# Performance work log

Measured on AMD Instinct MI355X. Metric: run time of the kernel, lower is better.

## Reference

```python
import jax, jax.numpy as jnp
import numpy as np

GRAPH_SIZES = [864, 1728, 3456, 6912]
VERTEX_NUM = 6890
B, NZ, FC_DIM = 128, 128, 512
CH = [128, 128, 64, 32, 16]
EDGE_FACTOR = 6  # directed edges per node (triangle mesh)
LRELU = 0.2


def setup_inputs() -> dict:
    key = jax.random.key(0)
    ks = jax.random.split(key, 24)
    s = 0.02
    inp = {
        'x': jax.random.normal(ks[0], (B, NZ), jnp.float32),
        'fc_w1': s * jax.random.normal(ks[1], (NZ, FC_DIM), jnp.float32),
        'fc_b1': jnp.zeros((FC_DIM,), jnp.float32),
        'fc_w2': s * jax.random.normal(ks[2], (FC_DIM, GRAPH_SIZES[0] * CH[0]), jnp.float32),
        'fc_b2': jnp.zeros((GRAPH_SIZES[0] * CH[0],), jnp.float32),
    }
    # Chebyshev weights [K=3, C_in, C_out] per layer (+ final conv to 3)
    cio = [(CH[0], CH[1]), (CH[1], CH[2]), (CH[2], CH[3]), (CH[3], CH[4]), (CH[4], 3)]
    for i, (ci, co) in enumerate(cio):
        inp[f'W{i}'] = s * jax.random.normal(ks[3 + i], (3, ci, co), jnp.float32)
        inp[f'b{i}'] = jnp.zeros((co,), jnp.float32)
    # fixed edge lists per level
    for i, n in enumerate(GRAPH_SIZES):
        e = EDGE_FACTOR * n
        inp[f'edge{i}'] = jax.random.randint(ks[10 + i], (2, e), 0, n, dtype=jnp.int64)
    inp['perm_back'] = jax.random.randint(ks[20], (GRAPH_SIZES[-1],), 0, GRAPH_SIZES[-1], dtype=jnp.int64)
    return inp


def cheb_conv(x, edge_index, W, b, num_nodes):
    # PyG-style ChebConv with lambda_max=2: L_hat = L - I = -D^{-1/2} A D^{-1/2}
    src, dst = edge_index[0], edge_index[1]
    deg = jnp.zeros((num_nodes,), x.dtype).at[dst].add(jnp.ones(src.shape, x.dtype))
    dinv = jnp.where(deg > 0, 1.0 / jnp.sqrt(jnp.maximum(deg, 1.0)), 0.0)
    norm = -(dinv[src] * dinv[dst])  # [E]

    def prop(h):  # h: [B, N, C] -> L_hat @ h (gather + scatter-add over edges)
        msg = h[:, src, :] * norm[None, :, None]
        return jnp.zeros_like(h).at[:, dst, :].add(msg)

    Tx0 = x
    Tx1 = prop(Tx0)
    Tx2 = 2.0 * prop(Tx1) - Tx0
    out = (jnp.einsum('bnc,co->bno', Tx0, W[0])
           + jnp.einsum('bnc,co->bno', Tx1, W[1])
           + jnp.einsum('bnc,co->bno', Tx2, W[2]))
    return out + b


def lrelu(x):
    return jnp.where(x >= 0, x, LRELU * x)


def reference(x, fc_w1, fc_b1, fc_w2, fc_b2,
              W0, b0, W1, b1, W2, b2, W3, b3, W4, b4,
              edge0, edge1, edge2, edge3, perm_back):
    h = jax.nn.relu(x @ fc_w1 + fc_b1)
    h = h @ fc_w2 + fc_b2                      # dropout = identity (eval mode)
    h = h.reshape(h.shape[0], GRAPH_SIZES[0], -1)  # [B, 864, 128]
    edges = [edge0, edge1, edge2, edge3]
    Ws = [(W0, b0), (W1, b1), (W2, b2), (W3, b3)]
    for i in range(4):
        h = lrelu(cheb_conv(h, edges[i], Ws[i][0], Ws[i][1], GRAPH_SIZES[i]))
        if i < 3:
            h = jnp.repeat(h, 2, axis=1)       # Upsample(scale_factor=2) along nodes
    h = cheb_conv(h, edge3, W4, b4, GRAPH_SIZES[3])  # final conv to 3 coords
    h = h[:, perm_back, :]                      # perm_data gather
    return h[:, :VERTEX_NUM, :]
```

## Files before the change

### kernel.cpp

```cpp
#include <hip/hip_runtime.h>
#include <hip/hip_bf16.h>

#define DEVFN __device__ __forceinline__

__global__ void k_signal(float* out, float v) {
    if (threadIdx.x == 0 && blockIdx.x == 0) out[0] = v;
}

__global__ void k_detect64(const long long* __restrict__ p, int count, int* flag) {
    if (threadIdx.x == 0 && blockIdx.x == 0) {
        int ok = 1;
        for (int i = 0; i < count; i++) {
            long long v = p[i];
            if (v < 0 || v >= (1LL << 30)) { ok = 0; break; }
        }
        *flag = ok;
    }
}

__global__ __launch_bounds__(256) void k_cvt_idx(const void* __restrict__ p, int n,
                                                 const int* __restrict__ flag,
                                                 int* __restrict__ out) {
    int i = blockIdx.x * 256 + threadIdx.x;
    if (i >= n) return;
    if (*flag) out[i] = (int)((const long long*)p)[i];
    else       out[i] = ((const int*)p)[i];
}

__global__ __launch_bounds__(256) void k_fc1(const float* __restrict__ x,
                                             const float* __restrict__ w,
                                             const float* __restrict__ b,
                                             float* __restrict__ out) {
    int j = blockIdx.x * 256 + threadIdx.x;
    int m = blockIdx.y;
    float acc = b[j];
    const float* xr = x + m * 128;
    for (int k = 0; k < 128; k++)
        acc = fmaf(xr[k], w[k * 512 + j], acc);
    out[m * 512 + j] = fmaxf(acc, 0.f);
}

__global__ __launch_bounds__(256) void k_fc2_gemm3(const float* __restrict__ h1,
                                                   const float* __restrict__ w,
                                                   const float* __restrict__ bias,
                                                   float* __restrict__ out) {
    const int N = 110592, K = 512;
    constexpr int KT = 32, MT = 128, NT = 64, AST = 37;
    __shared__ float At[MT * AST];
    __shared__ float Bt[KT * NT];

    const int tid = threadIdx.x;
    const int cg = tid & 7;
    const int rg = tid >> 3;
    const int nbase = blockIdx.x * NT;
    const int c0 = cg * 8;

    float acc[4][8];
#pragma unroll
    for (int jj = 0; jj < 8; jj++) {
        float bj = bias[nbase + c0 + jj];
#pragma unroll
        for (int r = 0; r < 4; r++) acc[r][jj] = bj;
    }

    for (int k0 = 0; k0 < K; k0 += KT) {
        __syncthreads();
#pragma unroll
        for (int it = 0; it < 4; it++) {
            int idx = tid + it * 256;
            int row = idx >> 3, k4 = (idx & 7) * 4;
            float4 a = *(const float4*)(h1 + row * K + k0 + k4);
            float* dst = At + row * AST + k4;
            dst[0] = a.x; dst[1] = a.y; dst[2] = a.z; dst[3] = a.w;
        }
#pragma unroll
        for (int it = 0; it < 2; it++) {
            int idx = tid + it * 256;
            int kk = idx >> 4, c4 = (idx & 15) * 4;
            *(float4*)(Bt + kk * NT + c4) =
                *(const float4*)(w + (size_t)(k0 + kk) * N + nbase + c4);
        }
        __syncthreads();
#pragma unroll 4
        for (int k = 0; k < KT; k++) {
            float a0 = At[(rg * 4 + 0) * AST + k];
            float a1 = At[(rg * 4 + 1) * AST + k];
            float a2 = At[(rg * 4 + 2) * AST + k];
            float a3 = At[(rg * 4 + 3) * AST + k];
            float4 w0 = *(const float4*)(Bt + k * NT + c0);
            float4 w1 = *(const float4*)(Bt + k * NT + c0 + 4);
            float wv[8] = {w0.x, w0.y, w0.z, w0.w, w1.x, w1.y, w1.z, w1.w};
#pragma unroll
            for (int jj = 0; jj < 8; jj++) {
                acc[0][jj] = fmaf(a0, wv[jj], acc[0][jj]);
                acc[1][jj] = fmaf(a1, wv[jj], acc[1][jj]);
                acc[2][jj] = fmaf(a2, wv[jj], acc[2][jj]);
                acc[3][jj] = fmaf(a3, wv[jj], acc[3][jj]);
            }
        }
    }
#pragma unroll
    for (int r = 0; r < 4; r++) {
        int m = rg * 4 + r;
        float4 o0 = {acc[r][0], acc[r][1], acc[r][2], acc[r][3]};
        float4 o1 = {acc[r][4], acc[r][5], acc[r][6], acc[r][7]};
        *(float4*)(out + (size_t)m * N + nbase + c0) = o0;
        *(float4*)(out + (size_t)m * N + nbase + c0 + 4) = o1;
    }
}

__global__ __launch_bounds__(256) void k_zero_int(int* p, int n) {
    int i = blockIdx.x * 256 + threadIdx.x;
    if (i < n) p[i] = 0;
}

__global__ __launch_bounds__(256) void k_deg(const int* __restrict__ dst, int e,
                                             int* __restrict__ deg) {
    int i = blockIdx.x * 256 + threadIdx.x;
    if (i < e) atomicAdd(&deg[dst[i]], 1);
}

__global__ __launch_bounds__(256) void k_dinv(const int* __restrict__ deg,
                                              float* __restrict__ dinv, int n) {
    int i = blockIdx.x * 256 + threadIdx.x;
    if (i < n) dinv[i] = deg[i] > 0 ? 1.0f / sqrtf((float)deg[i]) : 0.0f;
}

__global__ __launch_bounds__(256) void k_scan(const int* __restrict__ deg,
                                              int* __restrict__ row_ptr, int n) {
    __shared__ int part[256];
    int tid = threadIdx.x;
    int per = (n + 255) / 256;
    int start = tid * per;
    int end = min(start + per, n);
    int s = 0;
    for (int i = start; i < end; i++) s += deg[i];
    part[tid] = s;
    __syncthreads();
    for (int off = 1; off < 256; off <<= 1) {
        int t = (tid >= off) ? part[tid - off] : 0;
        __syncthreads();
        part[tid] += t;
        __syncthreads();
    }
    int base = (tid == 0) ? 0 : part[tid - 1];
    int run = base;
    for (int i = start; i < end; i++) { row_ptr[i] = run; run += deg[i]; }
    if (tid == 255) row_ptr[n] = part[255];
}

__global__ __launch_bounds__(256) void k_fill(const int* __restrict__ src,
                                              const int* __restrict__ dst, int e,
                                              const int* __restrict__ row_ptr,
                                              int* __restrict__ cnt,
                                              const float* __restrict__ dinv,
                                              int* __restrict__ col, float* __restrict__ val) {
    int i = blockIdx.x * 256 + threadIdx.x;
    if (i >= e) return;
    int d = dst[i], s = src[i];
    int slot = row_ptr[d] + atomicAdd(&cnt[d], 1);
    col[slot] = s;
    val[slot] = -dinv[s] * dinv[d];
}

template <int CI, int MODE>
__global__ __launch_bounds__(256) void k_prop2(const float* __restrict__ h,
                                               const float* __restrict__ sub,
                                               const int* __restrict__ row_ptr,
                                               const int* __restrict__ col,
                                               const float* __restrict__ val,
                                               float* __restrict__ out, int n) {
    constexpr int C4 = CI / 4;
    constexpr int BY = 256 / C4;
    int c4 = threadIdx.x;
    int d = blockIdx.x;
    int b = blockIdx.y * BY + threadIdx.y;
    int p0 = row_ptr[d], p1 = row_ptr[d + 1];
    float4 acc = {0.f, 0.f, 0.f, 0.f};
    const float4* hb = (const float4*)h + (size_t)b * n * C4;
    for (int p = p0; p < p1; p++) {
        float vp = val[p];
        float4 hv = hb[(size_t)col[p] * C4 + c4];
        acc.x = fmaf(vp, hv.x, acc.x);
        acc.y = fmaf(vp, hv.y, acc.y);
        acc.z = fmaf(vp, hv.z, acc.z);
        acc.w = fmaf(vp, hv.w, acc.w);
    }
    size_t oi = ((size_t)b * n + d) * C4 + c4;
    if (MODE) {
        float4 s = ((const float4*)sub)[oi];
        acc.x = 2.f * acc.x - s.x;
        acc.y = 2.f * acc.y - s.y;
        acc.z = 2.f * acc.z - s.z;
        acc.w = 2.f * acc.w - s.w;
    }
    ((float4*)out)[oi] = acc;
}

template <int CI, int CO, bool REPEAT>
__global__ __launch_bounds__(256) void k_cheb_gemm3(const float* __restrict__ t0,
                                                    const float* __restrict__ t1,
                                                    const float* __restrict__ t2,
                                                    const float* __restrict__ W,
                                                    const float* __restrict__ bias,
                                                    float* __restrict__ out, int n) {
    constexpr int CGN = CO / 8;
    constexpr int MT = 1024 / CGN;
    constexpr int KT = 32, AST = 37;
    __shared__ float At[MT * AST];
    __shared__ float Wt_s[KT * CO];

    const int tid = threadIdx.x;
    const int cg = tid % CGN;
    const int rg = tid / CGN;
    const int m_base = blockIdx.x * MT;
    const int c0 = cg * 8;

    float acc[4][8];
#pragma unroll
    for (int jj = 0; jj < 8; jj++) {
        float bj = bias[c0 + jj];
#pragma unroll
        for (int r = 0; r < 4; r++) acc[r][jj] = bj;
    }

    const float* As[3] = {t0, t1, t2};
#pragma unroll 1
    for (int t = 0; t < 3; t++) {
        const float* A = As[t];
        const float* Wg = W + t * CI * CO;
#pragma unroll 1
        for (int k0 = 0; k0 < CI; k0 += KT) {
            __syncthreads();
#pragma unroll
            for (int it = 0; it < MT / 32; it++) {
                int idx = tid + it * 256;
                int row = idx >> 3, k4 = (idx & 7) * 4;
                float4 a = *(const float4*)(A + (size_t)(m_base + row) * CI + k0 + k4);
                float* dst = At + row * AST + k4;
                dst[0] = a.x; dst[1] = a.y; dst[2] = a.z; dst[3] = a.w;
            }
#pragma unroll
            for (int it = 0; it < (KT * CO) / 1024; it++) {
                int idx = tid + it * 256;
                int kk = idx / (CO / 4), c4 = (idx % (CO / 4)) * 4;
                *(float4*)(Wt_s + kk * CO + c4) =
                    *(const float4*)(Wg + (k0 + kk) * CO + c4);
            }
            __syncthreads();
#pragma unroll 4
            for (int k = 0; k < KT; k++) {
                float a0 = At[(rg * 4 + 0) * AST + k];
                float a1 = At[(rg * 4 + 1) * AST + k];
                float a2 = At[(rg * 4 + 2) * AST + k];
                float a3 = At[(rg * 4 + 3) * AST + k];
                float4 w0 = *(const float4*)(Wt_s + k * CO + c0);
                float4 w1 = *(const float4*)(Wt_s + k * CO + c0 + 4);
                float wv[8] = {w0.x, w0.y, w0.z, w0.w, w1.x, w1.y, w1.z, w1.w};
#pragma unroll
                for (int jj = 0; jj < 8; jj++) {
                    acc[0][jj] = fmaf(a0, wv[jj], acc[0][jj]);
                    acc[1][jj] = fmaf(a1, wv[jj], acc[1][jj]);
                    acc[2][jj] = fmaf(a2, wv[jj], acc[2][jj]);
                    acc[3][jj] = fmaf(a3, wv[jj], acc[3][jj]);
                }
            }
        }
    }

#pragma unroll
    for (int r = 0; r < 4; r++) {
        int m = m_base + rg * 4 + r;
#pragma unroll
        for (int jj = 0; jj < 8; jj++) {
            float v = acc[r][jj];
            acc[r][jj] = v >= 0.f ? v : 0.2f * v;
        }
        float4 o0 = {acc[r][0], acc[r][1], acc[r][2], acc[r][3]};
        float4 o1 = {acc[r][4], acc[r][5], acc[r][6], acc[r][7]};
        if (REPEAT) {
            int b = m / n, d = m - (m / n) * n;
            size_t ob = ((size_t)b * (2 * n) + 2 * d) * CO + c0;
            *(float4*)(out + ob) = o0;
            *(float4*)(out + ob + 4) = o1;
            *(float4*)(out + ob + CO) = o0;
            *(float4*)(out + ob + CO + 4) = o1;
        } else {
            *(float4*)(out + (size_t)m * CO + c0) = o0;
            *(float4*)(out + (size_t)m * CO + c0 + 4) = o1;
        }
    }
}

__global__ __launch_bounds__(256) void k_cheb_small(const float* __restrict__ t0,
                                                    const float* __restrict__ t1,
                                                    const float* __restrict__ t2,
                                                    const float* __restrict__ W,
                                                    const float* __restrict__ bias,
                                                    float* __restrict__ out) {
    constexpr int CI = 32, CO = 16, MT = 256, AST = 33;
    __shared__ float At[MT * AST];
    __shared__ float Ws[3 * CI * CO];

    const int tid = threadIdx.x;
    const int cg = tid & 1;
    const int rg = tid >> 1;
    const int c0 = cg * 8;
    const int m_base = blockIdx.x * MT;

    for (int i = tid; i < 384; i += 256)
        ((float4*)Ws)[i] = ((const float4*)W)[i];

    float acc[2][8];
#pragma unroll
    for (int jj = 0; jj < 8; jj++) {
        float bj = bias[c0 + jj];
        acc[0][jj] = bj; acc[1][jj] = bj;
    }

    const float* As[3] = {t0, t1, t2};
#pragma unroll 1
    for (int t = 0; t < 3; t++) {
        const float* A = As[t];
        __syncthreads();
#pragma unroll
        for (int it = 0; it < 8; it++) {
            int idx = tid + it * 256;
            int row = idx >> 3, k4 = (idx & 7) * 4;
            float4 a = *(const float4*)(A + (size_t)(m_base + row) * CI + k4);
            float* dst = At + row * AST + k4;
            dst[0] = a.x; dst[1] = a.y; dst[2] = a.z; dst[3] = a.w;
        }
        __syncthreads();
        const float* Wt = Ws + t * CI * CO;
#pragma unroll 8
        for (int k = 0; k < CI; k++) {
            float a0 = At[rg * AST + k];
            float a1 = At[(rg + 128) * AST + k];
            float4 w0 = *(const float4*)(Wt + k * CO + c0);
            float4 w1 = *(const float4*)(Wt + k * CO + c0 + 4);
            float wv[8] = {w0.x, w0.y, w0.z, w0.w, w1.x, w1.y, w1.z, w1.w};
#pragma unroll
            for (int jj = 0; jj < 8; jj++) {
                acc[0][jj] = fmaf(a0, wv[jj], acc[0][jj]);
                acc[1][jj] = fmaf(a1, wv[jj], acc[1][jj]);
            }
        }
    }

#pragma unroll
    for (int r = 0; r < 2; r++) {
        int m = m_base + rg + r * 128;
#pragma unroll
        for (int jj = 0; jj < 8; jj++) {
            float v = acc[r][jj];
            acc[r][jj] = v >= 0.f ? v : 0.2f * v;
        }
        float4 o0 = {acc[r][0], acc[r][1], acc[r][2], acc[r][3]};
        float4 o1 = {acc[r][4], acc[r][5], acc[r][6], acc[r][7]};
        *(float4*)(out + (size_t)m * CO + c0) = o0;
        *(float4*)(out + (size_t)m * CO + c0 + 4) = o1;
    }
}

__global__ __launch_bounds__(256) void k_final_conv(const float* __restrict__ t0,
                                                    const float* __restrict__ t1,
                                                    const float* __restrict__ t2,
                                                    const float* __restrict__ W,
                                                    const float* __restrict__ bias,
                                                    float* __restrict__ out, int M) {
    int m = blockIdx.x * 256 + threadIdx.x;
    if (m >= M) return;
    float a0 = bias[0], a1 = bias[1], a2 = bias[2];
    const float* hs[3] = {t0, t1, t2};
#pragma unroll
    for (int t = 0; t < 3; t++) {
        const float4* h4 = (const float4*)(hs[t] + (size_t)m * 16);
        const float* Wt = W + t * 48;
#pragma unroll
        for (int q = 0; q < 4; q++) {
            float4 hv = h4[q];
            const float* Wq = Wt + q * 12;
            a0 = fmaf(hv.x, Wq[0], a0); a1 = fmaf(hv.x, Wq[1], a1); a2 = fmaf(hv.x, Wq[2], a2);
            a0 = fmaf(hv.y, Wq[3], a0); a1 = fmaf(hv.y, Wq[4], a1); a2 = fmaf(hv.y, Wq[5], a2);
            a0 = fmaf(hv.z, Wq[6], a0); a1 = fmaf(hv.z, Wq[7], a1); a2 = fmaf(hv.z, Wq[8], a2);
            a0 = fmaf(hv.w, Wq[9], a0); a1 = fmaf(hv.w, Wq[10], a1); a2 = fmaf(hv.w, Wq[11], a2);
        }
    }
    out[(size_t)m * 3 + 0] = a0;
    out[(size_t)m * 3 + 1] = a1;
    out[(size_t)m * 3 + 2] = a2;
}

__global__ __launch_bounds__(256) void k_permute(const float* __restrict__ h,
                                                 const int* __restrict__ perm,
                                                 float* __restrict__ out) {
    const int V = 6890, N = 6912;
    int idx = blockIdx.x * 256 + threadIdx.x;
    if (idx >= 128 * V * 3) return;
    int c = idx % 3;
    int t = idx / 3;
    int v = t % V;
    int b = t / V;
    int p = perm[v];
    out[idx] = h[((size_t)b * N + p) * 3 + c];
}

extern "C" void kernel_launch(void* const* d_in, const int* in_sizes, int n_in,
                              void* d_out, int out_size, void* d_ws, size_t ws_size,
                              hipStream_t stream) {
    float* out = (float*)d_out;

    static const int SIZES[20] = {
        16384, 65536, 512, 56623104, 110592,
        49152, 128, 24576, 64, 6144, 32, 1536, 16, 144, 3,
        10368, 20736, 41472, 82944, 6912
    };
    const void* in[20];
    bool map_ok = (n_in == 20);
    if (map_ok) {
        for (int s = 0; s < 20; s++) {
            int found = -1;
            for (int i = 0; i < n_in; i++)
                if (in_sizes[i] == SIZES[s]) { found = i; break; }
            if (found < 0) { map_ok = false; break; }
            in[s] = d_in[found];
        }
    }
    if (!map_ok)
        for (int i = 0; i < 20 && i < n_in; i++) in[i] = d_in[i];

    const float* x     = (const float*)in[0];
    const float* fc_w1 = (const float*)in[1];
    const float* fc_b1 = (const float*)in[2];
    const float* fc_w2 = (const float*)in[3];
    const float* fc_b2 = (const float*)in[4];
    const float* W0 = (const float*)in[5];
    const float* b0 = (const float*)in[6];
    const float* W1 = (const float*)in[7];
    const float* b1 = (const float*)in[8];
    const float* W2 = (const float*)in[9];
    const float* b2 = (const float*)in[10];
    const float* W3 = (const float*)in[11];
    const float* b3 = (const float*)in[12];
    const float* W4 = (const float*)in[13];
    const float* b4 = (const float*)in[14];

    const size_t SZ = 28311552;
    float* ws = (float*)d_ws;
    float* buf0 = ws;
    float* buf1 = ws + SZ;
    float* buf2 = ws + 2 * SZ;
    float* buf3 = ws + 3 * SZ;
    float* h1   = ws + 4 * SZ;
    float* dinv = h1 + 65536;
    float* val  = dinv + 6912;
    int* ideg = (int*)(val + 41472);
    int* rowp = ideg + 6912;
    int* cnt  = rowp + 6913;
    int* col  = cnt + 6912;
    int* e0 = col + 41472;
    int* e1 = e0 + 10368;
    int* e2 = e1 + 20736;
    int* e3 = e2 + 41472;
    int* pm = e3 + 82944;
    int* flag = pm + 6912;
    size_t needed = (char*)(flag + 1) - (char*)d_ws;
    if (ws_size < needed) {
        k_signal<<<1, 64, 0, stream>>>(out, 1000.0f);
        return;
    }

    k_detect64<<<1, 64, 0, stream>>>((const long long*)in[15], 64, flag);
    k_cvt_idx<<<(10368 + 255) / 256, 256, 0, stream>>>(in[15], 10368, flag, e0);
    k_cvt_idx<<<(20736 + 255) / 256, 256, 0, stream>>>(in[16], 20736, flag, e1);
    k_cvt_idx<<<(41472 + 255) / 256, 256, 0, stream>>>(in[17], 41472, flag, e2);
    k_cvt_idx<<<(82944 + 255) / 256, 256, 0, stream>>>(in[18], 82944, flag, e3);
    k_cvt_idx<<<(6912 + 255) / 256, 256, 0, stream>>>(in[19], 6912, flag, pm);

    k_fc1<<<dim3(2, 128), 256, 0, stream>>>(x, fc_w1, fc_b1, h1);
    k_fc2_gemm3<<<1728, 256, 0, stream>>>(h1, fc_w2, fc_b2, buf0);

    auto build = [&](const int* edge, int e, int n) {
        int nb_n = (n + 255) / 256, nb_e = (e + 255) / 256;
        k_zero_int<<<nb_n, 256, 0, stream>>>(ideg, n);
        k_zero_int<<<nb_n, 256, 0, stream>>>(cnt, n);
        k_deg<<<nb_e, 256, 0, stream>>>(edge + e, e, ideg);
        k_dinv<<<nb_n, 256, 0, stream>>>(ideg, dinv, n);
        k_scan<<<1, 256, 0, stream>>>(ideg, rowp, n);
        k_fill<<<nb_e, 256, 0, stream>>>(edge, edge + e, e, rowp, cnt, dinv, col, val);
    };

    build(e0, 6 * 864, 864);
    k_prop2<128, 0><<<dim3(864, 16), dim3(32, 8), 0, stream>>>(buf0, buf0, rowp, col, val, buf1, 864);
    k_prop2<128, 1><<<dim3(864, 16), dim3(32, 8), 0, stream>>>(buf1, buf0, rowp, col, val, buf2, 864);
    k_cheb_gemm3<128, 128, true><<<1728, 256, 0, stream>>>(buf0, buf1, buf2, W0, b0, buf3, 864);

    build(e1, 6 * 1728, 1728);
    k_prop2<128, 0><<<dim3(1728, 16), dim3(32, 8), 0, stream>>>(buf3, buf3, rowp, col, val, buf1, 1728);
    k_prop2<128, 1><<<dim3(1728, 16), dim3(32, 8), 0, stream>>>(buf1, buf3, rowp, col, val, buf2, 1728);
    k_cheb_gemm3<128, 64, true><<<1728, 256, 0, stream>>>(buf3, buf1, buf2, W1, b1, buf0, 1728);

    build(e2, 6 * 3456, 3456);
    k_prop2<64, 0><<<dim3(3456, 8), dim3(16, 16), 0, stream>>>(buf0, buf0, rowp, col, val, buf1, 3456);
    k_prop2<64, 1><<<dim3(3456, 8), dim3(16, 16), 0, stream>>>(buf1, buf0, rowp, col, val, buf2, 3456);
    k_cheb_gemm3<64, 32, true><<<1728, 256, 0, stream>>>(buf0, buf1, buf2, W2, b2, buf3, 3456);

    build(e3, 6 * 6912, 6912);
    k_prop2<32, 0><<<dim3(6912, 4), dim3(8, 32), 0, stream>>>(buf3, buf3, rowp, col, val, buf1, 6912);
    k_prop2<32, 1><<<dim3(6912, 4), dim3(8, 32), 0, stream>>>(buf1, buf3, rowp, col, val, buf2, 6912);
    k_cheb_small<<<3456, 256, 0, stream>>>(buf3, buf1, buf2, W3, b3, buf0);

    k_prop2<16, 0><<<dim3(6912, 2), dim3(4, 64), 0, stream>>>(buf0, buf0, rowp, col, val, buf1, 6912);
    k_prop2<16, 1><<<dim3(6912, 2), dim3(4, 64), 0, stream>>>(buf1, buf0, rowp, col, val, buf2, 6912);
    k_final_conv<<<(884736 + 255) / 256, 256, 0, stream>>>(buf0, buf1, buf2, W4, b4, buf3, 884736);

    int tot = 128 * 6890 * 3;
    k_permute<<<(tot + 255) / 256, 256, 0, stream>>>(buf3, pm, out);

    if (!map_ok) k_signal<<<1, 64, 0, stream>>>(out, 2000.0f);
}
```

Baseline: 2.055 ms.

## Transpose fc1 output and use 8x8 register tiles in fc2 GEMM

fc1 now writes its activations transposed (K-major), so the fc2 GEMM can load A tiles with plain float4 copies instead of padded scalar stores. The fc2 kernel moves from a 4x8 to an 8x8 per-thread register tile, widens the N tile from 64 to 128 and halves the grid. This raises FMA work per shared-memory load and halves how often the A matrix is re-read across blocks. In exchange it uses more registers per thread, which may lower occupancy, and launches fewer blocks.

```diff
diff --git a/kernel.cpp b/kernel.cpp
--- a/kernel.cpp
+++ b/kernel.cpp
@@ -37,30 +37,32 @@
     const float* xr = x + m * 128;
     for (int k = 0; k < 128; k++)
         acc = fmaf(xr[k], w[k * 512 + j], acc);
-    out[m * 512 + j] = fmaxf(acc, 0.f);
-}
-
-__global__ __launch_bounds__(256) void k_fc2_gemm3(const float* __restrict__ h1,
+    out[j * 128 + m] = fmaxf(acc, 0.f);
+}
+
+__global__ __launch_bounds__(256) void k_fc2_gemm4(const float* __restrict__ h1t,
                                                    const float* __restrict__ w,
                                                    const float* __restrict__ bias,
                                                    float* __restrict__ out) {
     const int N = 110592, K = 512;
-    constexpr int KT = 32, MT = 128, NT = 64, AST = 37;
-    __shared__ float At[MT * AST];
+    constexpr int KT = 32, NT = 128;
+    __shared__ float At[KT * 128];
     __shared__ float Bt[KT * NT];
 
     const int tid = threadIdx.x;
-    const int cg = tid & 7;
-    const int rg = tid >> 3;
+    const int cg = tid & 15;
+    const int rg = tid >> 4;
     const int nbase = blockIdx.x * NT;
-    const int c0 = cg * 8;
-
-    float acc[4][8];
-#pragma unroll
-    for (int jj = 0; jj < 8; jj++) {
-        float bj = bias[nbase + c0 + jj];
-#pragma unroll
-        for (int r = 0; r < 4; r++) acc[r][jj] = bj;
+    const int r0 = rg * 8;
+    const int c0 = cg * 4;
+
+    float acc[8][8];
+#pragma unroll
+    for (int j = 0; j < 4; j++) {
+        float bj0 = bias[nbase + c0 + j];
+        float bj1 = bias[nbase + 64 + c0 + j];
+#pragma unroll
+        for (int r = 0; r < 8; r++) { acc[r][j] = bj0; acc[r][j + 4] = bj1; }
     }
 
     for (int k0 = 0; k0 < K; k0 += KT) {
@@ -68,44 +70,41 @@
 #pragma unroll
         for (int it = 0; it < 4; it++) {
             int idx = tid + it * 256;
-            int row = idx >> 3, k4 = (idx & 7) * 4;
-            float4 a = *(const float4*)(h1 + row * K + k0 + k4);
-            float* dst = At + row * AST + k4;
-            dst[0] = a.x; dst[1] = a.y; dst[2] = a.z; dst[3] = a.w;
-        }
-#pragma unroll
-        for (int it = 0; it < 2; it++) {
+            int kk = idx >> 5, r4 = (idx & 31) * 4;
+            *(float4*)(At + kk * 128 + r4) =
+                *(const float4*)(h1t + (size_t)(k0 + kk) * 128 + r4);
+        }
+#pragma unroll
+        for (int it = 0; it < 4; it++) {
             int idx = tid + it * 256;
-            int kk = idx >> 4, c4 = (idx & 15) * 4;
+            int kk = idx >> 5, c4 = (idx & 31) * 4;
             *(float4*)(Bt + kk * NT + c4) =
                 *(const float4*)(w + (size_t)(k0 + kk) * N + nbase + c4);
         }
         __syncthreads();
-#pragma unroll 4
+#pragma unroll 8
         for (int k = 0; k < KT; k++) {
-            float a0 = At[(rg * 4 + 0) * AST + k];
-            float a1 = At[(rg * 4 + 1) * AST + k];
-            float a2 = At[(rg * 4 + 2) * AST + k];
-            float a3 = At[(rg * 4 + 3) * AST + k];
-            float4 w0 = *(const float4*)(Bt + k * NT + c0);
-            float4 w1 = *(const float4*)(Bt + k * NT + c0 + 4);
-            float wv[8] = {w0.x, w0.y, w0.z, w0.w, w1.x, w1.y, w1.z, w1.w};
-#pragma unroll
-            for (int jj = 0; jj < 8; jj++) {
-                acc[0][jj] = fmaf(a0, wv[jj], acc[0][jj]);
-                acc[1][jj] = fmaf(a1, wv[jj], acc[1][jj]);
-                acc[2][jj] = fmaf(a2, wv[jj], acc[2][jj]);
-                acc[3][jj] = fmaf(a3, wv[jj], acc[3][jj]);
-            }
-        }
-    }
-#pragma unroll
-    for (int r = 0; r < 4; r++) {
-        int m = rg * 4 + r;
+            float4 a0 = *(const float4*)(At + k * 128 + r0);
+            float4 a1 = *(const float4*)(At + k * 128 + r0 + 4);
+            float4 b0 = *(const float4*)(Bt + k * NT + c0);
+            float4 b1 = *(const float4*)(Bt + k * NT + c0 + 64);
+            float av[8] = {a0.x, a0.y, a0.z, a0.w, a1.x, a1.y, a1.z, a1.w};
+            float bv[8] = {b0.x, b0.y, b0.z, b0.w, b1.x, b1.y, b1.z, b1.w};
+#pragma unroll
+            for (int r = 0; r < 8; r++)
+#pragma unroll
+                for (int j = 0; j < 8; j++)
+                    acc[r][j] = fmaf(av[r], bv[j], acc[r][j]);
+        }
+    }
+
+#pragma unroll
+    for (int r = 0; r < 8; r++) {
+        int m = r0 + r;
         float4 o0 = {acc[r][0], acc[r][1], acc[r][2], acc[r][3]};
         float4 o1 = {acc[r][4], acc[r][5], acc[r][6], acc[r][7]};
         *(float4*)(out + (size_t)m * N + nbase + c0) = o0;
-        *(float4*)(out + (size_t)m * N + nbase + c0 + 4) = o1;
+        *(float4*)(out + (size_t)m * N + nbase + c0 + 64) = o1;
     }
 }
 
@@ -479,7 +478,7 @@
     k_cvt_idx<<<(6912 + 255) / 256, 256, 0, stream>>>(in[19], 6912, flag, pm);
 
     k_fc1<<<dim3(2, 128), 256, 0, stream>>>(x, fc_w1, fc_b1, h1);
-    k_fc2_gemm3<<<1728, 256, 0, stream>>>(h1, fc_w2, fc_b2, buf0);
+    k_fc2_gemm4<<<864, 256, 0, stream>>>(h1, fc_w2, fc_b2, buf0);
 
     auto build = [&](const int* edge, int e, int n) {
         int nb_n = (n + 255) / 256, nb_e = (e + 255) / 256;
```

New measurement: 2.068 ms. No clear change (+0.6%).

## Reorder Chebyshev conv to project channels before graph propagation

Applied to the files above, without the earlier changes.

For layers 1-3, the Chebyshev conv is rewritten so the dense weight projection (X·W0, X·W1, X·W2) runs first. The two sparse propagations then act on the narrower output channels, with a fused combine kernel that adds bias, applies LeakyReLU and upsamples. Because propagation is linear, the result is unchanged, and the gather/scatter traffic scales with C_out instead of C_in. It adds a combined B/C buffer layout and a new GEMM kernel that keeps three accumulator sets, which raises register pressure.

```diff
diff --git a/kernel.cpp b/kernel.cpp
--- a/kernel.cpp
+++ b/kernel.cpp
@@ -292,12 +292,94 @@
     }
 }
 
-__global__ __launch_bounds__(256) void k_cheb_small(const float* __restrict__ t0,
-                                                    const float* __restrict__ t1,
-                                                    const float* __restrict__ t2,
-                                                    const float* __restrict__ W,
-                                                    const float* __restrict__ bias,
-                                                    float* __restrict__ out) {
+template <int CI, int CO>
+__global__ __launch_bounds__(256) void k_cheb_gemmABC(const float* __restrict__ t0,
+                                                      const float* __restrict__ W,
+                                                      const float* __restrict__ bias,
+                                                      float* __restrict__ outA,
+                                                      float* __restrict__ outBC) {
+    constexpr int CGN = CO / 8;
+    constexpr int MT = 1024 / CGN;
+    constexpr int KT = 32, AST = 37;
+    __shared__ float At[MT * AST];
+    __shared__ float Ws[3 * KT * CO];
+
+    const int tid = threadIdx.x;
+    const int cg = tid % CGN;
+    const int rg = tid / CGN;
+    const int m_base = blockIdx.x * MT;
+    const int c0 = cg * 8;
+
+    float acc[3][4][8] = {};
+
+#pragma unroll 1
+    for (int k0 = 0; k0 < CI; k0 += KT) {
+        __syncthreads();
+#pragma unroll
+        for (int it = 0; it < MT / 32; it++) {
+            int idx = tid + it * 256;
+            int row = idx >> 3, k4 = (idx & 7) * 4;
+            float4 a = *(const float4*)(t0 + (size_t)(m_base + row) * CI + k0 + k4);
+            float* dst = At + row * AST + k4;
+            dst[0] = a.x; dst[1] = a.y; dst[2] = a.z; dst[3] = a.w;
+        }
+#pragma unroll
+        for (int t = 0; t < 3; t++)
+#pragma unroll
+            for (int it = 0; it < CO / 32; it++) {
+                int idx = tid + it * 256;
+                int kk = idx / (CO / 4), c4 = (idx % (CO / 4)) * 4;
+                *(float4*)(Ws + t * KT * CO + kk * CO + c4) =
+                    *(const float4*)(W + t * CI * CO + (size_t)(k0 + kk) * CO + c4);
+            }
+        __syncthreads();
+#pragma unroll 2
+        for (int k = 0; k < KT; k++) {
+            float a0 = At[(rg * 4 + 0) * AST + k];
+            float a1 = At[(rg * 4 + 1) * AST + k];
+            float a2 = At[(rg * 4 + 2) * AST + k];
+            float a3 = At[(rg * 4 + 3) * AST + k];
+#pragma unroll
+            for (int t = 0; t < 3; t++) {
+                float4 w0 = *(const float4*)(Ws + t * KT * CO + k * CO + c0);
+                float4 w1 = *(const float4*)(Ws + t * KT * CO + k * CO + c0 + 4);
+                float wv[8] = {w0.x, w0.y, w0.z, w0.w, w1.x, w1.y, w1.z, w1.w};
+#pragma unroll
+                for (int jj = 0; jj < 8; jj++) {
+                    acc[t][0][jj] = fmaf(a0, wv[jj], acc[t][0][jj]);
+                    acc[t][1][jj] = fmaf(a1, wv[jj], acc[t][1][jj]);
+                    acc[t][2][jj] = fmaf(a2, wv[jj], acc[t][2][jj]);
+                    acc[t][3][jj] = fmaf(a3, wv[jj], acc[t][3][jj]);
+                }
+            }
+        }
+    }
+
+#pragma unroll
+    for (int r = 0; r < 4; r++) {
+        size_t m = m_base + rg * 4 + r;
+        float av[8], bv[8], cv[8];
+#pragma unroll
+        for (int jj = 0; jj < 8; jj++) {
+            cv[jj] = acc[2][r][jj];
+            av[jj] = acc[0][r][jj] - cv[jj] + bias[c0 + jj];
+            bv[jj] = acc[1][r][jj];
+        }
+        *(float4*)(outA + m * CO + c0)     = (float4){av[0], av[1], av[2], av[3]};
+        *(float4*)(outA + m * CO + c0 + 4) = (float4){av[4], av[5], av[6], av[7]};
+        float* bc = outBC + m * 2 * CO;
+        *(float4*)(bc + c0)          = (float4){bv[0], bv[1], bv[2], bv[3]};
+        *(float4*)(bc + c0 + 4)      = (float4){bv[4], bv[5], bv[6], bv[7]};
+        *(float4*)(bc + CO + c0)     = (float4){cv[0], cv[1], cv[2], cv[3]};
+        *(float4*)(bc + CO + c0 + 4) = (float4){cv[4], cv[5], cv[6], cv[7]};
+    }
+}
+
+__global__ __launch_bounds__(256) void k_cheb_smallABC(const float* __restrict__ t0,
+                                                       const float* __restrict__ W,
+                                                       const float* __restrict__ bias,
+                                                       float* __restrict__ outA,
+                                                       float* __restrict__ outBC) {
     constexpr int CI = 32, CO = 16, MT = 256, AST = 33;
     __shared__ float At[MT * AST];
     __shared__ float Ws[3 * CI * CO];
@@ -311,55 +393,95 @@
     for (int i = tid; i < 384; i += 256)
         ((float4*)Ws)[i] = ((const float4*)W)[i];
 
-    float acc[2][8];
-#pragma unroll
-    for (int jj = 0; jj < 8; jj++) {
-        float bj = bias[c0 + jj];
-        acc[0][jj] = bj; acc[1][jj] = bj;
-    }
-
-    const float* As[3] = {t0, t1, t2};
-#pragma unroll 1
-    for (int t = 0; t < 3; t++) {
-        const float* A = As[t];
-        __syncthreads();
-#pragma unroll
-        for (int it = 0; it < 8; it++) {
-            int idx = tid + it * 256;
-            int row = idx >> 3, k4 = (idx & 7) * 4;
-            float4 a = *(const float4*)(A + (size_t)(m_base + row) * CI + k4);
-            float* dst = At + row * AST + k4;
-            dst[0] = a.x; dst[1] = a.y; dst[2] = a.z; dst[3] = a.w;
-        }
-        __syncthreads();
-        const float* Wt = Ws + t * CI * CO;
-#pragma unroll 8
-        for (int k = 0; k < CI; k++) {
-            float a0 = At[rg * AST + k];
-            float a1 = At[(rg + 128) * AST + k];
-            float4 w0 = *(const float4*)(Wt + k * CO + c0);
-            float4 w1 = *(const float4*)(Wt + k * CO + c0 + 4);
+#pragma unroll
+    for (int it = 0; it < 8; it++) {
+        int idx = tid + it * 256;
+        int row = idx >> 3, k4 = (idx & 7) * 4;
+        float4 a = *(const float4*)(t0 + (size_t)(m_base + row) * CI + k4);
+        float* dst = At + row * AST + k4;
+        dst[0] = a.x; dst[1] = a.y; dst[2] = a.z; dst[3] = a.w;
+    }
+    __syncthreads();
+
+    float acc[3][2][8] = {};
+#pragma unroll 4
+    for (int k = 0; k < CI; k++) {
+        float a0 = At[rg * AST + k];
+        float a1 = At[(rg + 128) * AST + k];
+#pragma unroll
+        for (int t = 0; t < 3; t++) {
+            float4 w0 = *(const float4*)(Ws + t * CI * CO + k * CO + c0);
+            float4 w1 = *(const float4*)(Ws + t * CI * CO + k * CO + c0 + 4);
             float wv[8] = {w0.x, w0.y, w0.z, w0.w, w1.x, w1.y, w1.z, w1.w};
 #pragma unroll
             for (int jj = 0; jj < 8; jj++) {
-                acc[0][jj] = fmaf(a0, wv[jj], acc[0][jj]);
-                acc[1][jj] = fmaf(a1, wv[jj], acc[1][jj]);
+                acc[t][0][jj] = fmaf(a0, wv[jj], acc[t][0][jj]);
+                acc[t][1][jj] = fmaf(a1, wv[jj], acc[t][1][jj]);
             }
         }
     }
 
 #pragma unroll
     for (int r = 0; r < 2; r++) {
-        int m = m_base + rg + r * 128;
+        size_t m = m_base + rg + r * 128;
+        float av[8], bv[8], cv[8];
 #pragma unroll
         for (int jj = 0; jj < 8; jj++) {
-            float v = acc[r][jj];
-            acc[r][jj] = v >= 0.f ? v : 0.2f * v;
-        }
-        float4 o0 = {acc[r][0], acc[r][1], acc[r][2], acc[r][3]};
-        float4 o1 = {acc[r][4], acc[r][5], acc[r][6], acc[r][7]};
-        *(float4*)(out + (size_t)m * CO + c0) = o0;
-        *(float4*)(out + (size_t)m * CO + c0 + 4) = o1;
+            cv[jj] = acc[2][r][jj];
+            av[jj] = acc[0][r][jj] - cv[jj] + bias[c0 + jj];
+            bv[jj] = acc[1][r][jj];
+        }
+        *(float4*)(outA + m * CO + c0)     = (float4){av[0], av[1], av[2], av[3]};
+        *(float4*)(outA + m * CO + c0 + 4) = (float4){av[4], av[5], av[6], av[7]};
+        float* bc = outBC + m * 2 * CO;
+        *(float4*)(bc + c0)          = (float4){bv[0], bv[1], bv[2], bv[3]};
+        *(float4*)(bc + c0 + 4)      = (float4){bv[4], bv[5], bv[6], bv[7]};
+        *(float4*)(bc + CO + c0)     = (float4){cv[0], cv[1], cv[2], cv[3]};
+        *(float4*)(bc + CO + c0 + 4) = (float4){cv[4], cv[5], cv[6], cv[7]};
+    }
+}
+
+template <int CO, bool REPEAT>
+__global__ __launch_bounds__(256) void k_prop_comb(const float* __restrict__ pbc,
+                                                   const float* __restrict__ a,
+                                                   const int* __restrict__ row_ptr,
+                                                   const int* __restrict__ col,
+                                                   const float* __restrict__ val,
+                                                   float* __restrict__ out, int n) {
+    constexpr int C4 = CO / 4;
+    constexpr int BY = 256 / C4;
+    int c4 = threadIdx.x;
+    int d = blockIdx.x;
+    int b = blockIdx.y * BY + threadIdx.y;
+    int p0 = row_ptr[d], p1 = row_ptr[d + 1];
+    float4 acc = {0.f, 0.f, 0.f, 0.f};
+    const float4* pb4 = (const float4*)pbc + (size_t)b * n * (2 * C4);
+    for (int p = p0; p < p1; p++) {
+        float vp = val[p];
+        float4 hv = pb4[(size_t)col[p] * (2 * C4) + C4 + c4];
+        acc.x = fmaf(vp, hv.x, acc.x);
+        acc.y = fmaf(vp, hv.y, acc.y);
+        acc.z = fmaf(vp, hv.z, acc.z);
+        acc.w = fmaf(vp, hv.w, acc.w);
+    }
+    size_t node = (size_t)b * n + d;
+    float4 av = ((const float4*)a)[node * C4 + c4];
+    float4 pbv = pb4[(size_t)d * (2 * C4) + c4];
+    float4 f;
+    f.x = av.x + pbv.x + 2.f * acc.x;
+    f.y = av.y + pbv.y + 2.f * acc.y;
+    f.z = av.z + pbv.z + 2.f * acc.z;
+    f.w = av.w + pbv.w + 2.f * acc.w;
+    f.x = f.x >= 0.f ? f.x : 0.2f * f.x;
+    f.y = f.y >= 0.f ? f.y : 0.2f * f.y;
+    f.z = f.z >= 0.f ? f.z : 0.2f * f.z;
+    f.w = f.w >= 0.f ? f.w : 0.2f * f.w;
+    if (REPEAT) {
+        size_t o = ((size_t)b * 2 * n + 2 * d) * C4 + c4;
+        ((float4*)out)[o] = f;
+        ((float4*)out)[o + C4] = f;
+    } else {
+        ((float4*)out)[node * C4 + c4] = f;
     }
 }
 
@@ -497,26 +619,26 @@
     k_cheb_gemm3<128, 128, true><<<1728, 256, 0, stream>>>(buf0, buf1, buf2, W0, b0, buf3, 864);
 
     build(e1, 6 * 1728, 1728);
-    k_prop2<128, 0><<<dim3(1728, 16), dim3(32, 8), 0, stream>>>(buf3, buf3, rowp, col, val, buf1, 1728);
-    k_prop2<128, 1><<<dim3(1728, 16), dim3(32, 8), 0, stream>>>(buf1, buf3, rowp, col, val, buf2, 1728);
-    k_cheb_gemm3<128, 64, true><<<1728, 256, 0, stream>>>(buf3, buf1, buf2, W1, b1, buf0, 1728);
+    k_cheb_gemmABC<128, 64><<<1728, 256, 0, stream>>>(buf3, W1, b1, buf1, buf2);
+    k_prop2<128, 0><<<dim3(1728, 16), dim3(32, 8), 0, stream>>>(buf2, buf2, rowp, col, val, buf0, 1728);
+    k_prop_comb<64, true><<<dim3(1728, 8), dim3(16, 16), 0, stream>>>(buf0, buf1, rowp, col, val, buf3, 1728);
 
     build(e2, 6 * 3456, 3456);
-    k_prop2<64, 0><<<dim3(3456, 8), dim3(16, 16), 0, stream>>>(buf0, buf0, rowp, col, val, buf1, 3456);
-    k_prop2<64, 1><<<dim3(3456, 8), dim3(16, 16), 0, stream>>>(buf1, buf0, rowp, col, val, buf2, 3456);
-    k_cheb_gemm3<64, 32, true><<<1728, 256, 0, stream>>>(buf0, buf1, buf2, W2, b2, buf3, 3456);
+    k_cheb_gemmABC<64, 32><<<1728, 256, 0, stream>>>(buf3, W2, b2, buf1, buf2);
+    k_prop2<64, 0><<<dim3(3456, 8), dim3(16, 16), 0, stream>>>(buf2, buf2, rowp, col, val, buf0, 3456);
+    k_prop_comb<32, true><<<dim3(3456, 4), dim3(8, 32), 0, stream>>>(buf0, buf1, rowp, col, val, buf3, 3456);
 
     build(e3, 6 * 6912, 6912);
-    k_prop2<32, 0><<<dim3(6912, 4), dim3(8, 32), 0, stream>>>(buf3, buf3, rowp, col, val, buf1, 6912);
-    k_prop2<32, 1><<<dim3(6912, 4), dim3(8, 32), 0, stream>>>(buf1, buf3, rowp, col, val, buf2, 6912);
-    k_cheb_small<<<3456, 256, 0, stream>>>(buf3, buf1, buf2, W3, b3, buf0);
-
-    k_prop2<16, 0><<<dim3(6912, 2), dim3(4, 64), 0, stream>>>(buf0, buf0, rowp, col, val, buf1, 6912);
-    k_prop2<16, 1><<<dim3(6912, 2), dim3(4, 64), 0, stream>>>(buf1, buf0, rowp, col, val, buf2, 6912);
-    k_final_conv<<<(884736 + 255) / 256, 256, 0, stream>>>(buf0, buf1, buf2, W4, b4, buf3, 884736);
+    k_cheb_smallABC<<<3456, 256, 0, stream>>>(buf3, W3, b3, buf1, buf2);
+    k_prop2<32, 0><<<dim3(6912, 4), dim3(8, 32), 0, stream>>>(buf2, buf2, rowp, col, val, buf0, 6912);
+    k_prop_comb<16, false><<<dim3(6912, 2), dim3(4, 64), 0, stream>>>(buf0, buf1, rowp, col, val, buf3, 6912);
+
+    k_prop2<16, 0><<<dim3(6912, 2), dim3(4, 64), 0, stream>>>(buf3, buf3, rowp, col, val, buf1, 6912);
+    k_prop2<16, 1><<<dim3(6912, 2), dim3(4, 64), 0, stream>>>(buf1, buf3, rowp, col, val, buf2, 6912);
+    k_final_conv<<<(884736 + 255) / 256, 256, 0, stream>>>(buf3, buf1, buf2, W4, b4, buf0, 884736);
 
     int tot = 128 * 6890 * 3;
-    k_permute<<<(tot + 255) / 256, 256, 0, stream>>>(buf3, pm, out);
+    k_permute<<<(tot + 255) / 256, 256, 0, stream>>>(buf0, pm, out);
 
     if (!map_ok) k_signal<<<1, 64, 0, stream>>>(out, 2000.0f);
 }
```

Result: faster. 1.962 ms (-4.5%).
